# Performance work log

Measured on AMD Instinct MI355X. Metric: run time of the kernel, lower is better.

Reference implementation:

```python
import jax, jax.numpy as jnp
import numpy as np

N = 50000      # nodes
E = 800000     # edges in normalized A (incl. self loops)
DIN = 128      # input_dim
DOUT = 64      # output_dim
BN_EPS = 1e-5
SLOPE = 0.01   # LeakyReLU default negative slope


def setup_inputs() -> dict:
    key = jax.random.key(0)
    ks = jax.random.split(key, 10)
    H = jax.random.normal(ks[0], (N, DIN), dtype=jnp.float32)
    rows = jax.random.randint(ks[1], (E,), 0, N, dtype=jnp.int32)
    cols = jax.random.randint(ks[2], (E,), 0, N, dtype=jnp.int32)
    # values of the symmetrically normalized adjacency (precomputed in __init__)
    vals = jax.random.uniform(ks[3], (E,), dtype=jnp.float32)
    # BatchNorm1d params/buffers (eval mode: use running stats)
    gamma = 1.0 + 0.1 * jax.random.normal(ks[4], (DIN,), dtype=jnp.float32)
    beta = 0.1 * jax.random.normal(ks[5], (DIN,), dtype=jnp.float32)
    run_mean = 0.1 * jax.random.normal(ks[6], (DIN,), dtype=jnp.float32)
    run_var = 0.5 + jax.random.uniform(ks[7], (DIN,), dtype=jnp.float32)
    # Linear(input_dim, output_dim)
    W = jax.random.normal(ks[8], (DIN, DOUT), dtype=jnp.float32) / np.sqrt(DIN)
    b = 0.01 * jax.random.normal(ks[9], (DOUT,), dtype=jnp.float32)
    return dict(H=H, rows=rows, cols=cols, vals=vals, gamma=gamma, beta=beta,
                run_mean=run_mean, run_var=run_var, W=W, b=b)


def reference(H, rows, cols, vals, gamma, beta, run_mean, run_var, W, b):
    # F.normalize: L2 row normalization with eps=1e-12
    norm = jnp.maximum(jnp.linalg.norm(H, axis=1, keepdims=True), 1e-12)
    Hn = H / norm
    # BatchNorm1d (eval: running stats); dropout is identity in eval
    scale = gamma * jax.lax.rsqrt(run_var + BN_EPS)
    Hb = (Hn - run_mean) * scale + beta
    # Linear projection [N, DIN] @ [DIN, DOUT]
    X = Hb @ W + b
    # SpMM: out[r] = sum_{e: rows[e]==r} vals[e] * X[cols[e]]
    msgs = vals[:, None] * X[cols]            # [E, DOUT] gather + scale
    out = jax.ops.segment_sum(msgs, rows, num_segments=N)
    # LeakyReLU
    return jnp.where(out >= 0, out, SLOPE * out)
```

## Files before the change

### kernel.cpp

```cpp
#include <hip/hip_runtime.h>
#include <hip/hip_fp16.h>

#define N_NODES 50000
#define E_EDGES 800000
#define DIN 128
#define DOUT 64
#define NBUK 196
#define BUKCAP 4608
#define CHUNK 2048
#define NBLKA 391
#define NXP 391
#define NGRP 1563
#define GCAP 704
#define ASTRIDE 136
#define TILEB (64 * ASTRIDE * 2)

typedef short short8 __attribute__((ext_vector_type(8)));
typedef float f32x4 __attribute__((ext_vector_type(4)));

static __device__ __forceinline__ short f2bf(float f)
{
    union { float f; unsigned u; } x{f};
    const unsigned r = x.u + 0x7FFFu + ((x.u >> 16) & 1u);
    return (short)(r >> 16);
}

__global__ __launch_bounds__(512) void k_xa(
    const float* __restrict__ H, const float* __restrict__ gamma,
    const float* __restrict__ beta, const float* __restrict__ mean,
    const float* __restrict__ var, const float* __restrict__ W,
    const float* __restrict__ bias, unsigned short* __restrict__ X16,
    const int* __restrict__ rows, const int* __restrict__ cols,
    const float* __restrict__ vals, int* __restrict__ gcursor,
    unsigned* __restrict__ midVC, unsigned char* __restrict__ midR)
{
    __shared__ __align__(16) char smem[2][TILEB * 2];
    const int bid = blockIdx.x;
    const int t = threadIdx.x;

    if (bid < NBLKA) {
        int* lhist  = (int*)smem[0];
        int* lstart = lhist + 256;
        int* lcur   = lstart + 256;
        int* gbase  = lcur + 256;
        int* wsumS  = gbase + 256;
        unsigned* lbinVC = (unsigned*)(wsumS + 16);
        unsigned short* lbinBR = (unsigned short*)(lbinVC + CHUNK);

        const int lane = t & 63, wv = t >> 6;
        const int e0 = bid * CHUNK;
        const int nC = min(CHUNK, E_EDGES - e0);

        if (t < NBUK) lhist[t] = 0;
        __syncthreads();

        unsigned prVC[4];
        unsigned short prBR[4];
#pragma unroll
        for (int k = 0; k < 4; ++k) {
            const int e = e0 + k * 512 + t;
            if (e < E_EDGES) {
                const int r = rows[e];
                const unsigned hv = __half_as_ushort(__float2half(vals[e]));
                prVC[k] = (hv << 16) | (unsigned)cols[e];
                prBR[k] = (unsigned short)r;
                atomicAdd(&lhist[r >> 8], 1);
            } else {
                prBR[k] = 0xFFFFu;
            }
        }
        __syncthreads();

        const int v = (t < NBUK) ? lhist[t] : 0;
        int x = v;
        if (t < 256) {
#pragma unroll
            for (int o = 1; o < 64; o <<= 1) {
                const int y = __shfl_up(x, o, 64);
                if (lane >= o) x += y;
            }
            if (lane == 63) wsumS[wv] = x;
        }
        __syncthreads();
        if (t < NBUK) {
            int pre = 0;
            for (int i = 0; i < wv; ++i) pre += wsumS[i];
            const int ex = pre + x - v;
            lstart[t] = ex;
            lcur[t] = ex;
            gbase[t] = t * BUKCAP + (v ? atomicAdd(&gcursor[t], v) : 0);
        }
        __syncthreads();

#pragma unroll
        for (int k = 0; k < 4; ++k) {
            if (prBR[k] != 0xFFFFu) {
                const int bk = prBR[k] >> 8;
                const int pos = atomicAdd(&lcur[bk], 1);
                lbinVC[pos] = prVC[k];
                lbinBR[pos] = prBR[k];
            }
        }
        __syncthreads();

        for (int i = t; i < nC; i += 512) {
            const unsigned short br = lbinBR[i];
            const int bk = br >> 8;
            const int g = gbase[bk] + (i - lstart[bk]);
            if (g < (bk + 1) * BUKCAP) {
                midVC[g] = lbinVC[i];
                midR[g] = (unsigned char)(br & 255);
            }
        }
    } else {
        const int pair = bid - NBLKA;
        const int tile = t >> 8;
        const int tt = t & 255;
        short (*A_s)[ASTRIDE] = (short(*)[ASTRIDE])(smem[tile]);
        short (*B_s)[ASTRIDE] = (short(*)[ASTRIDE])(smem[tile] + TILEB);
        const int l = tt & 63, wv = tt >> 6;
        const int R0 = (pair * 2 + tile) * 64;

        {
            const int n = tt >> 2, koff = (tt & 3) * 32;
#pragma unroll
            for (int i = 0; i < 16; ++i) {
                const int k = koff + i * 2;
                const unsigned lo = (unsigned short)f2bf(W[k * DOUT + n]);
                const unsigned hi = (unsigned short)f2bf(W[(k + 1) * DOUT + n]);
                *(unsigned*)&B_s[n][k] = lo | (hi << 16);
            }
        }
        {
            const int rloc = tt >> 2, sub = tt & 3;
            const int r = R0 + rloc;
            float4 h[8];
            if (r < N_NODES) {
                const float4* hp = (const float4*)(H + (size_t)r * DIN + sub * 32);
#pragma unroll
                for (int i = 0; i < 8; ++i) h[i] = hp[i];
            } else {
#pragma unroll
                for (int i = 0; i < 8; ++i) h[i] = make_float4(0.f, 0.f, 0.f, 0.f);
            }
            float ss = 0.f;
#pragma unroll
            for (int i = 0; i < 8; ++i)
                ss += h[i].x * h[i].x + h[i].y * h[i].y + h[i].z * h[i].z + h[i].w * h[i].w;
            ss += __shfl_xor(ss, 1, 64);
            ss += __shfl_xor(ss, 2, 64);
            const float inv = 1.0f / fmaxf(sqrtf(ss), 1e-12f);

            const float4* gp = (const float4*)(gamma + sub * 32);
            const float4* bp = (const float4*)(beta  + sub * 32);
            const float4* mp = (const float4*)(mean  + sub * 32);
            const float4* vp = (const float4*)(var   + sub * 32);
#pragma unroll
            for (int i = 0; i < 8; ++i) {
                const float4 g4 = gp[i], b4 = bp[i], m4 = mp[i], v4 = vp[i];
                const float s0 = g4.x * rsqrtf(v4.x + 1e-5f);
                const float s1 = g4.y * rsqrtf(v4.y + 1e-5f);
                const float s2 = g4.z * rsqrtf(v4.z + 1e-5f);
                const float s3 = g4.w * rsqrtf(v4.w + 1e-5f);
                const float e0 = h[i].x * inv * s0 + (b4.x - m4.x * s0);
                const float e1 = h[i].y * inv * s1 + (b4.y - m4.y * s1);
                const float e2 = h[i].z * inv * s2 + (b4.z - m4.z * s2);
                const float e3 = h[i].w * inv * s3 + (b4.w - m4.w * s3);
                const unsigned u0 = (unsigned short)f2bf(e0) | ((unsigned)(unsigned short)f2bf(e1) << 16);
                const unsigned u1 = (unsigned short)f2bf(e2) | ((unsigned)(unsigned short)f2bf(e3) << 16);
                *(uint2*)&A_s[rloc][sub * 32 + i * 4] = make_uint2(u0, u1);
            }
        }

        const int ml = l & 15, q = l >> 4;
        f32x4 c0, c1, c2, c3;
        {
            const float b0 = bias[ml],      b1 = bias[16 + ml];
            const float b2 = bias[32 + ml], b3 = bias[48 + ml];
            c0 = f32x4{b0, b0, b0, b0};
            c1 = f32x4{b1, b1, b1, b1};
            c2 = f32x4{b2, b2, b2, b2};
            c3 = f32x4{b3, b3, b3, b3};
        }
        __syncthreads();

#pragma unroll
        for (int k0 = 0; k0 < 4; ++k0) {
            const short8 a  = *(const short8*)&A_s[wv * 16 + ml][k0 * 32 + q * 8];
            const short8 b0 = *(const short8*)&B_s[ml][k0 * 32 + q * 8];
            const short8 b1 = *(const short8*)&B_s[16 + ml][k0 * 32 + q * 8];
            const short8 b2 = *(const short8*)&B_s[32 + ml][k0 * 32 + q * 8];
            const short8 b3 = *(const short8*)&B_s[48 + ml][k0 * 32 + q * 8];
            c0 = __builtin_amdgcn_mfma_f32_16x16x32_bf16(a, b0, c0, 0, 0, 0);
            c1 = __builtin_amdgcn_mfma_f32_16x16x32_bf16(a, b1, c1, 0, 0, 0);
            c2 = __builtin_amdgcn_mfma_f32_16x16x32_bf16(a, b2, c2, 0, 0, 0);
            c3 = __builtin_amdgcn_mfma_f32_16x16x32_bf16(a, b3, c3, 0, 0, 0);
        }

        __syncthreads();
        unsigned short* otile = (unsigned short*)&A_s[0][0];
#pragma unroll
        for (int i = 0; i < 4; ++i) {
            const int r = wv * 16 + q * 4 + i;
            otile[r * 64 + ml]      = __half_as_ushort(__float2half(c0[i]));
            otile[r * 64 + 16 + ml] = __half_as_ushort(__float2half(c1[i]));
            otile[r * 64 + 32 + ml] = __half_as_ushort(__float2half(c2[i]));
            otile[r * 64 + 48 + ml] = __half_as_ushort(__float2half(c3[i]));
        }
        __syncthreads();
#pragma unroll
        for (int rep = 0; rep < 2; ++rep) {
            const int id = rep * 256 + tt;
            const int row = id >> 3;
            const int off = (id & 7) * 8;
            if (R0 + row < N_NODES)
                *(uint4*)(X16 + (size_t)(R0 + row) * DOUT + off) =
                    *(const uint4*)&otile[row * 64 + off];
        }
    }
}

__global__ __launch_bounds__(256) void k_passB(
    const int* __restrict__ gcursor, const unsigned* __restrict__ midVC,
    const unsigned char* __restrict__ midR, unsigned* __restrict__ ev,
    int2* __restrict__ rowSE)
{
    __shared__ int lhist[32], lcur[32];
    const int g  = blockIdx.x;
    const int bk = g >> 3;
    const int q  = g & 7;
    const int base = bk * BUKCAP;
    const int total = min(gcursor[bk], BUKCAP);
    const int t = threadIdx.x;

    if (t < 32) lhist[t] = 0;
    __syncthreads();
    for (int i = t; i < total; i += 256) {
        const int lr = midR[base + i];
        if ((lr >> 5) == q) atomicAdd(&lhist[lr & 31], 1);
    }
    __syncthreads();
    if (t < 32) {
        const int v = lhist[t];
        int x = v;
#pragma unroll
        for (int o = 1; o < 32; o <<= 1) {
            const int y = __shfl_up(x, o, 64);
            if (t >= o) x += y;
        }
        const int ex = x - v;
        lcur[t] = min(ex, GCAP);
        const int row = (g << 5) | t;
        if (row < N_NODES)
            rowSE[row] = make_int2(g * GCAP + min(ex, GCAP),
                                   g * GCAP + min(ex + v, GCAP));
    }
    __syncthreads();
    for (int i = t; i < total; i += 256) {
        const int lr = midR[base + i];
        if ((lr >> 5) == q) {
            const int pos = atomicAdd(&lcur[lr & 31], 1);
            if (pos < GCAP) ev[g * GCAP + pos] = midVC[base + i];
        }
    }
}

__global__ __launch_bounds__(256) void k_spmm(
    const int2* __restrict__ rowSE, const unsigned* __restrict__ ev,
    const unsigned short* __restrict__ X16, float* __restrict__ out)
{
    const int lane = threadIdx.x & 63;
    const int hl   = lane & 31;
    const int h    = lane >> 5;
    const int row  = blockIdx.x * 4 + (threadIdx.x >> 6);
    const int2 se = rowSE[row];
    const int s = se.x, e2 = se.y;
    float ax = 0.f, ay = 0.f;
    for (int c = s; c < e2; c += 64) {
        const int idx = c + lane;
        unsigned p = 0;
        if (idx < e2) p = ev[idx];
        const int cnt  = min(e2 - c, 64);
        const int jmax = (cnt + 1) >> 1;
        int j = 0;
        for (; j + 1 < jmax; j += 2) {
            const unsigned u0 = (unsigned)__shfl((int)p, 2 * j + h,     64);
            const unsigned u1 = (unsigned)__shfl((int)p, 2 * j + 2 + h, 64);
            const unsigned x0 = *(const unsigned*)(X16 + (u0 & 0xFFFFu) * DOUT + 2 * hl);
            const unsigned x1 = *(const unsigned*)(X16 + (u1 & 0xFFFFu) * DOUT + 2 * hl);
            const float v0 = __half2float(__ushort_as_half((unsigned short)(u0 >> 16)));
            const float v1 = __half2float(__ushort_as_half((unsigned short)(u1 >> 16)));
            const float2 f0 = __half22float2(*(const __half2*)&x0);
            const float2 f1 = __half22float2(*(const __half2*)&x1);
            ax = fmaf(v0, f0.x, ax); ay = fmaf(v0, f0.y, ay);
            ax = fmaf(v1, f1.x, ax); ay = fmaf(v1, f1.y, ay);
        }
        for (; j < jmax; ++j) {
            const unsigned u = (unsigned)__shfl((int)p, 2 * j + h, 64);
            const unsigned x = *(const unsigned*)(X16 + (u & 0xFFFFu) * DOUT + 2 * hl);
            const float v = __half2float(__ushort_as_half((unsigned short)(u >> 16)));
            const float2 f = __half22float2(*(const __half2*)&x);
            ax = fmaf(v, f.x, ax); ay = fmaf(v, f.y, ay);
        }
    }
    ax += __shfl_xor(ax, 32, 64);
    ay += __shfl_xor(ay, 32, 64);
    if (h == 0) {
        float2 r;
        r.x = (ax >= 0.f) ? ax : 0.01f * ax;
        r.y = (ay >= 0.f) ? ay : 0.01f * ay;
        *(float2*)(out + (size_t)row * DOUT + 2 * hl) = r;
    }
}

extern "C" void kernel_launch(void* const* d_in, const int* in_sizes, int n_in,
                              void* d_out, int out_size, void* d_ws, size_t ws_size,
                              hipStream_t stream)
{
    const float* H     = (const float*)d_in[0];
    const int*   rows  = (const int*)  d_in[1];
    const int*   cols  = (const int*)  d_in[2];
    const float* vals  = (const float*)d_in[3];
    const float* gamma = (const float*)d_in[4];
    const float* beta  = (const float*)d_in[5];
    const float* mean  = (const float*)d_in[6];
    const float* var   = (const float*)d_in[7];
    const float* W     = (const float*)d_in[8];
    const float* bias  = (const float*)d_in[9];
    float* out = (float*)d_out;

    char* ws = (char*)d_ws;
    unsigned short* X16     = (unsigned short*)(ws);
    int*            gcursor = (int*)          (ws +  6400000);
    unsigned*       midVC   = (unsigned*)     (ws +  6400800);
    unsigned char*  midR    = (unsigned char*)(ws + 10013472);
    unsigned*       ev      = (unsigned*)     (ws + 10916640);
    int2*           rowSE   = (int2*)         (ws + 15318048);

    hipMemsetAsync(gcursor, 0, NBUK * sizeof(int), stream);
    k_xa<<<NBLKA + NXP, 512, 0, stream>>>(H, gamma, beta, mean, var, W, bias,
                                          X16, rows, cols, vals, gcursor,
                                          midVC, midR);
    k_passB<<<NGRP, 256, 0, stream>>>(gcursor, midVC, midR, ev, rowSE);
    k_spmm<<<N_NODES / 4, 256, 0, stream>>>(rowSE, ev, X16, out);
}
```

Before: 165.8 us.

## Split fused projection/bucketing kernel and fold cursor reset into projection kernel

Splits the combined kernel, where blocks either bucketed edges or computed two 64-row projection tiles, into two kernels. One is a 256-thread projection kernel with one tile per block; the other is a 512-thread edge bucketing kernel. The memset of the bucket cursors is removed and block 0 of the projection kernel zeroes them instead, dropping one API call. This adds a kernel launch boundary and gives up the overlap between projection and bucketing, in exchange for smaller per-block LDS and simpler blocks.

```diff
diff --git a/kernel.cpp b/kernel.cpp
--- a/kernel.cpp
+++ b/kernel.cpp
@@ -9,11 +9,9 @@
 #define BUKCAP 4608
 #define CHUNK 2048
 #define NBLKA 391
-#define NXP 391
 #define NGRP 1563
 #define GCAP 704
 #define ASTRIDE 136
-#define TILEB (64 * ASTRIDE * 2)
 
 typedef short short8 __attribute__((ext_vector_type(8)));
 typedef float f32x4 __attribute__((ext_vector_type(4)));
@@ -25,197 +23,192 @@
     return (short)(r >> 16);
 }
 
-__global__ __launch_bounds__(512) void k_xa(
+__global__ __launch_bounds__(256) void k_x(
     const float* __restrict__ H, const float* __restrict__ gamma,
     const float* __restrict__ beta, const float* __restrict__ mean,
     const float* __restrict__ var, const float* __restrict__ W,
     const float* __restrict__ bias, unsigned short* __restrict__ X16,
+    int* __restrict__ gcursor)
+{
+    __shared__ short A_s[64][ASTRIDE];
+    __shared__ short B_s[64][ASTRIDE];
+    const int t = threadIdx.x;
+    const int l = t & 63, wv = t >> 6;
+    const int R0 = blockIdx.x * 64;
+
+    if (blockIdx.x == 0 && t < NBUK) gcursor[t] = 0;
+
+    {
+        const int n = t >> 2, koff = (t & 3) * 32;
+#pragma unroll
+        for (int i = 0; i < 16; ++i) {
+            const int k = koff + i * 2;
+            const unsigned lo = (unsigned short)f2bf(W[k * DOUT + n]);
+            const unsigned hi = (unsigned short)f2bf(W[(k + 1) * DOUT + n]);
+            *(unsigned*)&B_s[n][k] = lo | (hi << 16);
+        }
+    }
+    {
+        const int rloc = t >> 2, sub = t & 3;
+        const int r = R0 + rloc;
+        float4 h[8];
+        if (r < N_NODES) {
+            const float4* hp = (const float4*)(H + (size_t)r * DIN + sub * 32);
+#pragma unroll
+            for (int i = 0; i < 8; ++i) h[i] = hp[i];
+        } else {
+#pragma unroll
+            for (int i = 0; i < 8; ++i) h[i] = make_float4(0.f, 0.f, 0.f, 0.f);
+        }
+        float ss = 0.f;
+#pragma unroll
+        for (int i = 0; i < 8; ++i)
+            ss += h[i].x * h[i].x + h[i].y * h[i].y + h[i].z * h[i].z + h[i].w * h[i].w;
+        ss += __shfl_xor(ss, 1, 64);
+        ss += __shfl_xor(ss, 2, 64);
+        const float inv = 1.0f / fmaxf(sqrtf(ss), 1e-12f);
+
+        const float4* gp = (const float4*)(gamma + sub * 32);
+        const float4* bp = (const float4*)(beta  + sub * 32);
+        const float4* mp = (const float4*)(mean  + sub * 32);
+        const float4* vp = (const float4*)(var   + sub * 32);
+#pragma unroll
+        for (int i = 0; i < 8; ++i) {
+            const float4 g4 = gp[i], b4 = bp[i], m4 = mp[i], v4 = vp[i];
+            const float s0 = g4.x * rsqrtf(v4.x + 1e-5f);
+            const float s1 = g4.y * rsqrtf(v4.y + 1e-5f);
+            const float s2 = g4.z * rsqrtf(v4.z + 1e-5f);
+            const float s3 = g4.w * rsqrtf(v4.w + 1e-5f);
+            const float e0 = h[i].x * inv * s0 + (b4.x - m4.x * s0);
+            const float e1 = h[i].y * inv * s1 + (b4.y - m4.y * s1);
+            const float e2 = h[i].z * inv * s2 + (b4.z - m4.z * s2);
+            const float e3 = h[i].w * inv * s3 + (b4.w - m4.w * s3);
+            const unsigned u0 = (unsigned short)f2bf(e0) | ((unsigned)(unsigned short)f2bf(e1) << 16);
+            const unsigned u1 = (unsigned short)f2bf(e2) | ((unsigned)(unsigned short)f2bf(e3) << 16);
+            *(uint2*)&A_s[rloc][sub * 32 + i * 4] = make_uint2(u0, u1);
+        }
+    }
+
+    const int ml = l & 15, q = l >> 4;
+    f32x4 c0, c1, c2, c3;
+    {
+        const float b0 = bias[ml],      b1 = bias[16 + ml];
+        const float b2 = bias[32 + ml], b3 = bias[48 + ml];
+        c0 = f32x4{b0, b0, b0, b0};
+        c1 = f32x4{b1, b1, b1, b1};
+        c2 = f32x4{b2, b2, b2, b2};
+        c3 = f32x4{b3, b3, b3, b3};
+    }
+    __syncthreads();
+
+#pragma unroll
+    for (int k0 = 0; k0 < 4; ++k0) {
+        const short8 a  = *(const short8*)&A_s[wv * 16 + ml][k0 * 32 + q * 8];
+        const short8 b0 = *(const short8*)&B_s[ml][k0 * 32 + q * 8];
+        const short8 b1 = *(const short8*)&B_s[16 + ml][k0 * 32 + q * 8];
+        const short8 b2 = *(const short8*)&B_s[32 + ml][k0 * 32 + q * 8];
+        const short8 b3 = *(const short8*)&B_s[48 + ml][k0 * 32 + q * 8];
+        c0 = __builtin_amdgcn_mfma_f32_16x16x32_bf16(a, b0, c0, 0, 0, 0);
+        c1 = __builtin_amdgcn_mfma_f32_16x16x32_bf16(a, b1, c1, 0, 0, 0);
+        c2 = __builtin_amdgcn_mfma_f32_16x16x32_bf16(a, b2, c2, 0, 0, 0);
+        c3 = __builtin_amdgcn_mfma_f32_16x16x32_bf16(a, b3, c3, 0, 0, 0);
+    }
+
+    __syncthreads();
+    unsigned short* otile = (unsigned short*)&A_s[0][0];
+#pragma unroll
+    for (int i = 0; i < 4; ++i) {
+        const int r = wv * 16 + q * 4 + i;
+        otile[r * 64 + ml]      = __half_as_ushort(__float2half(c0[i]));
+        otile[r * 64 + 16 + ml] = __half_as_ushort(__float2half(c1[i]));
+        otile[r * 64 + 32 + ml] = __half_as_ushort(__float2half(c2[i]));
+        otile[r * 64 + 48 + ml] = __half_as_ushort(__float2half(c3[i]));
+    }
+    __syncthreads();
+#pragma unroll
+    for (int rep = 0; rep < 2; ++rep) {
+        const int id = rep * 256 + t;
+        const int row = id >> 3;
+        const int off = (id & 7) * 8;
+        if (R0 + row < N_NODES)
+            *(uint4*)(X16 + (size_t)(R0 + row) * DOUT + off) =
+                *(const uint4*)&otile[row * 64 + off];
+    }
+}
+
+__global__ __launch_bounds__(512) void k_passA(
     const int* __restrict__ rows, const int* __restrict__ cols,
     const float* __restrict__ vals, int* __restrict__ gcursor,
     unsigned* __restrict__ midVC, unsigned char* __restrict__ midR)
 {
-    __shared__ __align__(16) char smem[2][TILEB * 2];
-    const int bid = blockIdx.x;
+    __shared__ int lhist[NBUK], lstart[NBUK], lcur[NBUK], gbase[NBUK];
+    __shared__ int wsumS[4];
+    __shared__ unsigned lbinVC[CHUNK];
+    __shared__ unsigned short lbinBR[CHUNK];
     const int t = threadIdx.x;
-
-    if (bid < NBLKA) {
-        int* lhist  = (int*)smem[0];
-        int* lstart = lhist + 256;
-        int* lcur   = lstart + 256;
-        int* gbase  = lcur + 256;
-        int* wsumS  = gbase + 256;
-        unsigned* lbinVC = (unsigned*)(wsumS + 16);
-        unsigned short* lbinBR = (unsigned short*)(lbinVC + CHUNK);
-
-        const int lane = t & 63, wv = t >> 6;
-        const int e0 = bid * CHUNK;
-        const int nC = min(CHUNK, E_EDGES - e0);
-
-        if (t < NBUK) lhist[t] = 0;
-        __syncthreads();
-
-        unsigned prVC[4];
-        unsigned short prBR[4];
-#pragma unroll
-        for (int k = 0; k < 4; ++k) {
-            const int e = e0 + k * 512 + t;
-            if (e < E_EDGES) {
-                const int r = rows[e];
-                const unsigned hv = __half_as_ushort(__float2half(vals[e]));
-                prVC[k] = (hv << 16) | (unsigned)cols[e];
-                prBR[k] = (unsigned short)r;
-                atomicAdd(&lhist[r >> 8], 1);
-            } else {
-                prBR[k] = 0xFFFFu;
-            }
-        }
-        __syncthreads();
-
-        const int v = (t < NBUK) ? lhist[t] : 0;
-        int x = v;
-        if (t < 256) {
-#pragma unroll
-            for (int o = 1; o < 64; o <<= 1) {
-                const int y = __shfl_up(x, o, 64);
-                if (lane >= o) x += y;
-            }
-            if (lane == 63) wsumS[wv] = x;
-        }
-        __syncthreads();
-        if (t < NBUK) {
-            int pre = 0;
-            for (int i = 0; i < wv; ++i) pre += wsumS[i];
-            const int ex = pre + x - v;
-            lstart[t] = ex;
-            lcur[t] = ex;
-            gbase[t] = t * BUKCAP + (v ? atomicAdd(&gcursor[t], v) : 0);
-        }
-        __syncthreads();
-
-#pragma unroll
-        for (int k = 0; k < 4; ++k) {
-            if (prBR[k] != 0xFFFFu) {
-                const int bk = prBR[k] >> 8;
-                const int pos = atomicAdd(&lcur[bk], 1);
-                lbinVC[pos] = prVC[k];
-                lbinBR[pos] = prBR[k];
-            }
-        }
-        __syncthreads();
-
-        for (int i = t; i < nC; i += 512) {
-            const unsigned short br = lbinBR[i];
-            const int bk = br >> 8;
-            const int g = gbase[bk] + (i - lstart[bk]);
-            if (g < (bk + 1) * BUKCAP) {
-                midVC[g] = lbinVC[i];
-                midR[g] = (unsigned char)(br & 255);
-            }
-        }
-    } else {
-        const int pair = bid - NBLKA;
-        const int tile = t >> 8;
-        const int tt = t & 255;
-        short (*A_s)[ASTRIDE] = (short(*)[ASTRIDE])(smem[tile]);
-        short (*B_s)[ASTRIDE] = (short(*)[ASTRIDE])(smem[tile] + TILEB);
-        const int l = tt & 63, wv = tt >> 6;
-        const int R0 = (pair * 2 + tile) * 64;
-
-        {
-            const int n = tt >> 2, koff = (tt & 3) * 32;
-#pragma unroll
-            for (int i = 0; i < 16; ++i) {
-                const int k = koff + i * 2;
-                const unsigned lo = (unsigned short)f2bf(W[k * DOUT + n]);
-                const unsigned hi = (unsigned short)f2bf(W[(k + 1) * DOUT + n]);
-                *(unsigned*)&B_s[n][k] = lo | (hi << 16);
-            }
-        }
-        {
-            const int rloc = tt >> 2, sub = tt & 3;
-            const int r = R0 + rloc;
-            float4 h[8];
-            if (r < N_NODES) {
-                const float4* hp = (const float4*)(H + (size_t)r * DIN + sub * 32);
-#pragma unroll
-                for (int i = 0; i < 8; ++i) h[i] = hp[i];
-            } else {
-#pragma unroll
-                for (int i = 0; i < 8; ++i) h[i] = make_float4(0.f, 0.f, 0.f, 0.f);
-            }
-            float ss = 0.f;
-#pragma unroll
-            for (int i = 0; i < 8; ++i)
-                ss += h[i].x * h[i].x + h[i].y * h[i].y + h[i].z * h[i].z + h[i].w * h[i].w;
-            ss += __shfl_xor(ss, 1, 64);
-            ss += __shfl_xor(ss, 2, 64);
-            const float inv = 1.0f / fmaxf(sqrtf(ss), 1e-12f);
-
-            const float4* gp = (const float4*)(gamma + sub * 32);
-            const float4* bp = (const float4*)(beta  + sub * 32);
-            const float4* mp = (const float4*)(mean  + sub * 32);
-            const float4* vp = (const float4*)(var   + sub * 32);
-#pragma unroll
-            for (int i = 0; i < 8; ++i) {
-                const float4 g4 = gp[i], b4 = bp[i], m4 = mp[i], v4 = vp[i];
-                const float s0 = g4.x * rsqrtf(v4.x + 1e-5f);
-                const float s1 = g4.y * rsqrtf(v4.y + 1e-5f);
-                const float s2 = g4.z * rsqrtf(v4.z + 1e-5f);
-                const float s3 = g4.w * rsqrtf(v4.w + 1e-5f);
-                const float e0 = h[i].x * inv * s0 + (b4.x - m4.x * s0);
-                const float e1 = h[i].y * inv * s1 + (b4.y - m4.y * s1);
-                const float e2 = h[i].z * inv * s2 + (b4.z - m4.z * s2);
-                const float e3 = h[i].w * inv * s3 + (b4.w - m4.w * s3);
-                const unsigned u0 = (unsigned short)f2bf(e0) | ((unsigned)(unsigned short)f2bf(e1) << 16);
-                const unsigned u1 = (unsigned short)f2bf(e2) | ((unsigned)(unsigned short)f2bf(e3) << 16);
-                *(uint2*)&A_s[rloc][sub * 32 + i * 4] = make_uint2(u0, u1);
-            }
-        }
-
-        const int ml = l & 15, q = l >> 4;
-        f32x4 c0, c1, c2, c3;
-        {
-            const float b0 = bias[ml],      b1 = bias[16 + ml];
-            const float b2 = bias[32 + ml], b3 = bias[48 + ml];
-            c0 = f32x4{b0, b0, b0, b0};
-            c1 = f32x4{b1, b1, b1, b1};
-            c2 = f32x4{b2, b2, b2, b2};
-            c3 = f32x4{b3, b3, b3, b3};
-        }
-        __syncthreads();
-
-#pragma unroll
-        for (int k0 = 0; k0 < 4; ++k0) {
-            const short8 a  = *(const short8*)&A_s[wv * 16 + ml][k0 * 32 + q * 8];
-            const short8 b0 = *(const short8*)&B_s[ml][k0 * 32 + q * 8];
-            const short8 b1 = *(const short8*)&B_s[16 + ml][k0 * 32 + q * 8];
-            const short8 b2 = *(const short8*)&B_s[32 + ml][k0 * 32 + q * 8];
-            const short8 b3 = *(const short8*)&B_s[48 + ml][k0 * 32 + q * 8];
-            c0 = __builtin_amdgcn_mfma_f32_16x16x32_bf16(a, b0, c0, 0, 0, 0);
-            c1 = __builtin_amdgcn_mfma_f32_16x16x32_bf16(a, b1, c1, 0, 0, 0);
-            c2 = __builtin_amdgcn_mfma_f32_16x16x32_bf16(a, b2, c2, 0, 0, 0);
-            c3 = __builtin_amdgcn_mfma_f32_16x16x32_bf16(a, b3, c3, 0, 0, 0);
-        }
-
-        __syncthreads();
-        unsigned short* otile = (unsigned short*)&A_s[0][0];
-#pragma unroll
-        for (int i = 0; i < 4; ++i) {
-            const int r = wv * 16 + q * 4 + i;
-            otile[r * 64 + ml]      = __half_as_ushort(__float2half(c0[i]));
-            otile[r * 64 + 16 + ml] = __half_as_ushort(__float2half(c1[i]));
-            otile[r * 64 + 32 + ml] = __half_as_ushort(__float2half(c2[i]));
-            otile[r * 64 + 48 + ml] = __half_as_ushort(__float2half(c3[i]));
-        }
-        __syncthreads();
-#pragma unroll
-        for (int rep = 0; rep < 2; ++rep) {
-            const int id = rep * 256 + tt;
-            const int row = id >> 3;
-            const int off = (id & 7) * 8;
-            if (R0 + row < N_NODES)
-                *(uint4*)(X16 + (size_t)(R0 + row) * DOUT + off) =
-                    *(const uint4*)&otile[row * 64 + off];
+    const int lane = t & 63, wv = t >> 6;
+    const int e0 = blockIdx.x * CHUNK;
+    const int nC = min(CHUNK, E_EDGES - e0);
+
+    if (t < NBUK) lhist[t] = 0;
+    __syncthreads();
+
+    unsigned prVC[4];
+    unsigned short prBR[4];
+#pragma unroll
+    for (int k = 0; k < 4; ++k) {
+        const int e = e0 + k * 512 + t;
+        if (e < E_EDGES) {
+            const int r = rows[e];
+            const unsigned hv = __half_as_ushort(__float2half(vals[e]));
+            prVC[k] = (hv << 16) | (unsigned)cols[e];
+            prBR[k] = (unsigned short)r;
+            atomicAdd(&lhist[r >> 8], 1);
+        } else {
+            prBR[k] = 0xFFFFu;
+        }
+    }
+    __syncthreads();
+
+    const int v = (t < NBUK) ? lhist[t] : 0;
+    int x = v;
+    if (t < 256) {
+#pragma unroll
+        for (int o = 1; o < 64; o <<= 1) {
+            const int y = __shfl_up(x, o, 64);
+            if (lane >= o) x += y;
+        }
+        if (lane == 63) wsumS[wv] = x;
+    }
+    __syncthreads();
+    if (t < NBUK) {
+        int pre = 0;
+        for (int i = 0; i < wv; ++i) pre += wsumS[i];
+        const int ex = pre + x - v;
+        lstart[t] = ex;
+        lcur[t] = ex;
+        gbase[t] = t * BUKCAP + (v ? atomicAdd(&gcursor[t], v) : 0);
+    }
+    __syncthreads();
+
+#pragma unroll
+    for (int k = 0; k < 4; ++k) {
+        if (prBR[k] != 0xFFFFu) {
+            const int bk = prBR[k] >> 8;
+            const int pos = atomicAdd(&lcur[bk], 1);
+            lbinVC[pos] = prVC[k];
+            lbinBR[pos] = prBR[k];
+        }
+    }
+    __syncthreads();
+
+    for (int i = t; i < nC; i += 512) {
+        const unsigned short br = lbinBR[i];
+        const int bk = br >> 8;
+        const int g = gbase[bk] + (i - lstart[bk]);
+        if (g < (bk + 1) * BUKCAP) {
+            midVC[g] = lbinVC[i];
+            midR[g] = (unsigned char)(br & 255);
         }
     }
 }
@@ -337,10 +330,9 @@
     unsigned*       ev      = (unsigned*)     (ws + 10916640);
     int2*           rowSE   = (int2*)         (ws + 15318048);
 
-    hipMemsetAsync(gcursor, 0, NBUK * sizeof(int), stream);
-    k_xa<<<NBLKA + NXP, 512, 0, stream>>>(H, gamma, beta, mean, var, W, bias,
-                                          X16, rows, cols, vals, gcursor,
-                                          midVC, midR);
+    k_x<<<(N_NODES + 63) / 64, 256, 0, stream>>>(H, gamma, beta, mean, var, W,
+                                                 bias, X16, gcursor);
+    k_passA<<<NBLKA, 512, 0, stream>>>(rows, cols, vals, gcursor, midVC, midR);
     k_passB<<<NGRP, 256, 0, stream>>>(gcursor, midVC, midR, ev, rowSE);
     k_spmm<<<N_NODES / 4, 256, 0, stream>>>(rowSE, ev, X16, out);
 }
```

New measurement: 166.9 us. Within noise of the previous version (+0.7%).
